# Performance work log

Hardware: AMD Instinct MI355X
Metric: run time of the kernel (lower is better)

The kernel has to match this reference:

```python
import jax, jax.numpy as jnp
import numpy as np

N_HEAD = 8
HEAD_DIM = 128
WINDOW = 512
ROPE_BASE = 10000.0


def _rope_tables(T, dtype):
    # inv_freq: [head_dim/2]
    inv_freq = 1.0 / (ROPE_BASE ** (jnp.arange(0, HEAD_DIM, 2, dtype=jnp.float32) / HEAD_DIM))
    t = jnp.arange(T, dtype=jnp.float32)
    freqs = jnp.einsum('i,j->ij', t, inv_freq)          # [T, head_dim/2]
    emb = jnp.concatenate([freqs, freqs], axis=-1)       # [T, head_dim]
    return jnp.cos(emb).astype(dtype), jnp.sin(emb).astype(dtype)


def _rotate_half(x):
    d = x.shape[-1] // 2
    return jnp.concatenate([-x[..., d:], x[..., :d]], axis=-1)


def setup_inputs() -> dict:
    key = jax.random.key(0)
    k1, k2, k3 = jax.random.split(key, 3)
    B, T, C = 2, 4096, 1024
    x = jax.random.normal(k1, (B, T, C), dtype=jnp.float32)
    w_qkv = jax.random.normal(k2, (3 * C, C), dtype=jnp.float32) * (1.0 / np.sqrt(C))
    w_o = jax.random.normal(k3, (C, C), dtype=jnp.float32) * (1.0 / np.sqrt(C))
    return {"x": x, "w_qkv": w_qkv, "w_o": w_o}


def reference(x, w_qkv, w_o):
    B, T, C = x.shape
    scale = 1.0 / np.sqrt(HEAD_DIM)
    qkv = x @ w_qkv.T                                     # [B,T,3C]
    q, k, v = jnp.split(qkv, 3, axis=-1)
    # [B, H, T, D]
    q = q.reshape(B, T, N_HEAD, HEAD_DIM).transpose(0, 2, 1, 3)
    k = k.reshape(B, T, N_HEAD, HEAD_DIM).transpose(0, 2, 1, 3)
    v = v.reshape(B, T, N_HEAD, HEAD_DIM).transpose(0, 2, 1, 3)
    cos, sin = _rope_tables(T, x.dtype)                   # [T, D]
    cos = cos[None, None]
    sin = sin[None, None]
    q = q * cos + _rotate_half(q) * sin
    k = k * cos + _rotate_half(k) * sin
    attn = jnp.einsum('bhqd,bhkd->bhqk', q, k) * scale    # [B,H,T,T]
    i = jnp.arange(T)[:, None]
    j = jnp.arange(T)[None, :]
    # causal (j<=i) AND sliding window triu(diag=-W) (j >= i - W)
    keep = (j <= i) & (j >= i - WINDOW)
    neg = jnp.finfo(attn.dtype).min
    attn = jnp.where(keep[None, None], attn, neg)
    attn = jax.nn.softmax(attn, axis=-1)
    out = jnp.einsum('bhqk,bhkd->bhqd', attn, v)          # [B,H,T,D]
    out = out.transpose(0, 2, 1, 3).reshape(B, T, C)
    return out @ w_o.T
```

## Files before the change

kernel.cpp:

```cpp
#include <hip/hip_runtime.h>
#include <hip/hip_bf16.h>

typedef unsigned short us;
typedef __attribute__((ext_vector_type(8))) __bf16 bf16x8;
typedef __attribute__((ext_vector_type(4))) float f32x4;

#define MFMA16(a, b, c) __builtin_amdgcn_mfma_f32_16x16x32_bf16(a, b, c, 0, 0, 0)

static __device__ __forceinline__ us f2bf(float f) {
  __hip_bfloat16 h = __float2bfloat16(f);
  return __builtin_bit_cast(us, h);
}

static __device__ __forceinline__ void gll16(const us* g, us* l) {
  __builtin_amdgcn_global_load_lds((const __attribute__((address_space(1))) void*)g,
                                   (__attribute__((address_space(3))) void*)l,
                                   16, 0, 0);
}

__global__ void cast_kernel(const float* __restrict__ in, us* __restrict__ out, int n4) {
  int i = blockIdx.x * blockDim.x + threadIdx.x;
  if (i >= n4) return;
  float4 v = ((const float4*)in)[i];
  ushort4 o;
  o.x = f2bf(v.x); o.y = f2bf(v.y); o.z = f2bf(v.z); o.w = f2bf(v.w);
  ((ushort4*)out)[i] = o;
}

__global__ void rope_table_kernel(float* __restrict__ ct, float* __restrict__ st) {
  int t = blockIdx.x, d = threadIdx.x;
  float ang = (float)t * exp2f((float)d * -0.20762050593046014f);
  float s, c;
  sincosf(ang, &s, &c);
  ct[t * 64 + d] = c;
  st[t * 64 + d] = s;
}

__global__ __launch_bounds__(256, 2)
void qkv_rope_kernel(const us* __restrict__ A, const us* __restrict__ B,
                     const float* __restrict__ ctab, const float* __restrict__ stab,
                     us* __restrict__ qb, us* __restrict__ kb, us* __restrict__ vtb) {
  __shared__ __align__(16) char smem_raw[128 * 132 * 4];
  us* sA = (us*)smem_raw;
  us* sB = sA + 128 * 64;
  float* sC = (float*)smem_raw;

  const int tid = threadIdx.x;
  const int lane = tid & 63;
  const int wave = tid >> 6;
  const int l15 = lane & 15;
  const int lq = lane >> 4;
  const int m0 = blockIdx.x * 128;
  const int n0 = blockIdx.y * 128;
  const int wm = (wave & 1) * 64;
  const int wn = (wave >> 1) * 64;

  f32x4 acc[4][4] = {};

  for (int k0 = 0; k0 < 1024; k0 += 64) {
    for (int i = 0; i < 4; ++i) {
      int c = wave * 4 + i;
      int P = c * 64 + lane;
      int row = P >> 3;
      int cb = (P & 7) ^ (row & 7);
      gll16(A + (size_t)(m0 + row) * 1024 + k0 + cb * 8, sA + c * 512);
      gll16(B + (size_t)(n0 + row) * 1024 + k0 + cb * 8, sB + c * 512);
    }
    __syncthreads();
#pragma unroll
    for (int kk = 0; kk < 64; kk += 32) {
      const int cbr = (kk + lq * 8) >> 3;
      bf16x8 av[4], bv[4];
#pragma unroll
      for (int mt = 0; mt < 4; ++mt) {
        int m = wm + mt * 16 + l15;
        av[mt] = *(const bf16x8*)(sA + (m * 8 + (cbr ^ (m & 7))) * 8);
      }
#pragma unroll
      for (int nt = 0; nt < 4; ++nt) {
        int n = wn + nt * 16 + l15;
        bv[nt] = *(const bf16x8*)(sB + (n * 8 + (cbr ^ (n & 7))) * 8);
      }
#pragma unroll
      for (int mt = 0; mt < 4; ++mt)
#pragma unroll
        for (int nt = 0; nt < 4; ++nt)
          acc[mt][nt] = MFMA16(av[mt], bv[nt], acc[mt][nt]);
    }
    __syncthreads();
  }

#pragma unroll
  for (int mt = 0; mt < 4; ++mt)
#pragma unroll
    for (int nt = 0; nt < 4; ++nt)
#pragma unroll
      for (int r = 0; r < 4; ++r) {
        int row = wm + mt * 16 + lq * 4 + r;
        int col = wn + nt * 16 + l15;
        sC[row * 132 + col] = acc[mt][nt][r];
      }
  __syncthreads();

  const int b = m0 >> 12;
  const int t0 = m0 & 4095;
  const int which = blockIdx.y >> 3;
  const int h = blockIdx.y & 7;

  if (which < 2) {
    us* outp = (which == 0) ? qb : kb;
    for (int r = 0; r < 8; ++r) {
      int tl = (tid >> 4) + r * 16;
      int d0 = (tid & 15) * 8;
      int tg = t0 + tl;
      int dm = d0 & 63;
      float cs[8], sn[8];
      *(float4*)(cs)     = *(const float4*)(ctab + tg * 64 + dm);
      *(float4*)(cs + 4) = *(const float4*)(ctab + tg * 64 + dm + 4);
      *(float4*)(sn)     = *(const float4*)(stab + tg * 64 + dm);
      *(float4*)(sn + 4) = *(const float4*)(stab + tg * 64 + dm + 4);
      union { us u[8]; uint4 v; } tmp;
#pragma unroll
      for (int j = 0; j < 8; ++j) {
        int d = d0 + j;
        float xv = sC[tl * 132 + d];
        float xp = sC[tl * 132 + (d ^ 64)];
        float rot = (d < 64) ? -xp : xp;
        tmp.u[j] = f2bf(xv * cs[j] + rot * sn[j]);
      }
      *(uint4*)(outp + ((size_t)((b * 8 + h) * 4096 + tg)) * 128 + d0) = tmp.v;
    }
  } else {
    for (int r = 0; r < 8; ++r) {
      int d = (tid >> 4) + r * 16;
      int tl0 = (tid & 15) * 8;
      union { us u[8]; uint4 v; } tmp;
#pragma unroll
      for (int j = 0; j < 8; ++j)
        tmp.u[j] = f2bf(sC[(tl0 + j) * 132 + d]);
      *(uint4*)(vtb + ((size_t)((b * 8 + h) * 128 + d)) * 4096 + t0 + tl0) = tmp.v;
    }
  }
}

template <int MASK>
__device__ __forceinline__ void softmax_step(f32x4 (&s)[8], f32x4 (&o)[8],
                                             float (&m_st)[4], float (&l_st)[4],
                                             us* __restrict__ sP,
                                             int t0, int tj0, int wm16, int lq, int l15) {
  const float C2 = 0.08838834764831845f * 1.4426950408889634f;
#pragma unroll
  for (int r = 0; r < 4; ++r) {
    const int rowl = wm16 + lq * 4 + r;
    const int ig = t0 + rowl;
    float mx = -3.0e38f;
#pragma unroll
    for (int nt = 0; nt < 8; ++nt) {
      float v = s[nt][r];
      if (MASK == 1) { int jg = tj0 + nt * 16 + l15; v = (jg + 512 >= ig) ? v : -3.0e38f; }
      if (MASK == 2) { int jg = tj0 + nt * 16 + l15; v = (jg <= ig) ? v : -3.0e38f; }
      s[nt][r] = v;
      mx = fmaxf(mx, v);
    }
#pragma unroll
    for (int off = 1; off < 16; off <<= 1) mx = fmaxf(mx, __shfl_xor(mx, off, 64));
    const float mold = m_st[r];
    const float mnew = fmaxf(mold, mx);
    const float alpha = exp2f((mold - mnew) * C2);
    float rs = 0.0f;
#pragma unroll
    for (int nt = 0; nt < 8; ++nt) {
      float p = exp2f((s[nt][r] - mnew) * C2);
      sP[rowl * 136 + nt * 16 + l15] = f2bf(p);
      rs += p;
    }
#pragma unroll
    for (int off = 1; off < 16; off <<= 1) rs += __shfl_xor(rs, off, 64);
    m_st[r] = mnew;
    l_st[r] = l_st[r] * alpha + rs;
#pragma unroll
    for (int dt = 0; dt < 8; ++dt) o[dt][r] *= alpha;
  }
}

__global__ __launch_bounds__(256, 2)
void flash_kernel(const us* __restrict__ qg, const us* __restrict__ kg,
                  const us* __restrict__ vg, us* __restrict__ ao) {
  __shared__ us sKP[128 * 128];
  __shared__ us sV[128 * 128];

  const int tid = threadIdx.x;
  const int lane = tid & 63;
  const int wave = tid >> 6;
  const int l15 = lane & 15;
  const int lq = lane >> 4;
  const int qx = blockIdx.x;
  const int h = blockIdx.y;
  const int b = blockIdx.z;
  const int t0 = qx * 64;
  const size_t bh = (size_t)(b * 8 + h);
  const int wm16 = wave * 16;

  bf16x8 qf[4];
#pragma unroll
  for (int ks = 0; ks < 4; ++ks)
    qf[ks] = *(const bf16x8*)(qg + (bh * 4096 + t0 + wm16 + l15) * 128 + ks * 32 + lq * 8);

  float m_st[4], l_st[4];
  f32x4 o[8] = {};
#pragma unroll
  for (int r = 0; r < 4; ++r) { m_st[r] = -3.0e38f; l_st[r] = 0.0f; }

  const int lo = t0 - 512;
  const int jtmin = (lo <= 0) ? 0 : (lo >> 7);
  const int jtmax = (t0 + 63) >> 7;
  const bool wmask = (t0 >= 512);

  for (int jt = jtmin; jt <= jtmax; ++jt) {
    const int tj0 = jt * 128;
    for (int i = 0; i < 8; ++i) {
      int c = wave * 8 + i;
      int P = c * 64 + lane;
      int row = P >> 4;
      int cb = (P & 15) ^ (row & 15);
      gll16(kg + (bh * 4096 + tj0 + row) * 128 + cb * 8, sKP + c * 512);
      gll16(vg + (bh * 128 + row) * 4096 + tj0 + cb * 8, sV + c * 512);
    }
    __syncthreads();

    f32x4 s[8] = {};
#pragma unroll
    for (int ks = 0; ks < 4; ++ks) {
      const int cbr = ks * 4 + lq;
#pragma unroll
      for (int nt = 0; nt < 8; ++nt) {
        int n = nt * 16 + l15;
        bf16x8 bk = *(const bf16x8*)(sKP + (n * 16 + (cbr ^ (n & 15))) * 8);
        s[nt] = MFMA16(qf[ks], bk, s[nt]);
      }
    }
    __syncthreads();

    if (jt == jtmax)               softmax_step<2>(s, o, m_st, l_st, sKP, t0, tj0, wm16, lq, l15);
    else if (wmask && jt == jtmin) softmax_step<1>(s, o, m_st, l_st, sKP, t0, tj0, wm16, lq, l15);
    else                           softmax_step<0>(s, o, m_st, l_st, sKP, t0, tj0, wm16, lq, l15);

#pragma unroll
    for (int ks = 0; ks < 4; ++ks) {
      const int ko = ks * 32 + lq * 8;
      const int cbr = ko >> 3;
      bf16x8 ap = *(const bf16x8*)(sKP + (wm16 + l15) * 136 + ko);
#pragma unroll
      for (int dt = 0; dt < 8; ++dt) {
        int dd = dt * 16 + l15;
        bf16x8 bv = *(const bf16x8*)(sV + (dd * 16 + (cbr ^ (dd & 15))) * 8);
        o[dt] = MFMA16(ap, bv, o[dt]);
      }
    }
    __syncthreads();
  }

#pragma unroll
  for (int r = 0; r < 4; ++r) {
    const float inv = 1.0f / l_st[r];
    const int rowl = wm16 + lq * 4 + r;
    const size_t base = ((size_t)b * 4096 + t0 + rowl) * 1024 + h * 128;
#pragma unroll
    for (int dt = 0; dt < 8; ++dt)
      ao[base + dt * 16 + l15] = f2bf(o[dt][r] * inv);
  }
}

__global__ __launch_bounds__(256, 2)
void out_proj_kernel(const us* __restrict__ A, const us* __restrict__ B, float* __restrict__ C) {
  __shared__ us sA[128 * 64];
  __shared__ us sB[128 * 64];
  const int tid = threadIdx.x;
  const int lane = tid & 63;
  const int wave = tid >> 6;
  const int l15 = lane & 15;
  const int lq = lane >> 4;
  const int m0 = blockIdx.x * 128;
  const int n0 = blockIdx.y * 128;
  const int wm = (wave & 1) * 64;
  const int wn = (wave >> 1) * 64;
  f32x4 acc[4][4] = {};
  for (int k0 = 0; k0 < 1024; k0 += 64) {
    for (int i = 0; i < 4; ++i) {
      int c = wave * 4 + i;
      int P = c * 64 + lane;
      int row = P >> 3;
      int cb = (P & 7) ^ (row & 7);
      gll16(A + (size_t)(m0 + row) * 1024 + k0 + cb * 8, sA + c * 512);
      gll16(B + (size_t)(n0 + row) * 1024 + k0 + cb * 8, sB + c * 512);
    }
    __syncthreads();
#pragma unroll
    for (int kk = 0; kk < 64; kk += 32) {
      const int cbr = (kk + lq * 8) >> 3;
      bf16x8 av[4], bv[4];
#pragma unroll
      for (int mt = 0; mt < 4; ++mt) {
        int m = wm + mt * 16 + l15;
        av[mt] = *(const bf16x8*)(sA + (m * 8 + (cbr ^ (m & 7))) * 8);
      }
#pragma unroll
      for (int nt = 0; nt < 4; ++nt) {
        int n = wn + nt * 16 + l15;
        bv[nt] = *(const bf16x8*)(sB + (n * 8 + (cbr ^ (n & 7))) * 8);
      }
#pragma unroll
      for (int mt = 0; mt < 4; ++mt)
#pragma unroll
        for (int nt = 0; nt < 4; ++nt)
          acc[mt][nt] = MFMA16(av[mt], bv[nt], acc[mt][nt]);
    }
    __syncthreads();
  }
#pragma unroll
  for (int mt = 0; mt < 4; ++mt)
#pragma unroll
    for (int nt = 0; nt < 4; ++nt)
#pragma unroll
      for (int r = 0; r < 4; ++r)
        C[(size_t)(m0 + wm + mt * 16 + lq * 4 + r) * 1024 + (n0 + wn + nt * 16 + l15)] =
            acc[mt][nt][r];
}

extern "C" void kernel_launch(void* const* d_in, const int* in_sizes, int n_in,
                              void* d_out, int out_size, void* d_ws, size_t ws_size,
                              hipStream_t stream) {
  const float* x     = (const float*)d_in[0];
  const float* w_qkv = (const float*)d_in[1];
  const float* w_o   = (const float*)d_in[2];
  float* out = (float*)d_out;

  us* xb  = (us*)d_ws;
  us* wqb = xb  + (size_t)8192 * 1024;
  us* wob = wqb + (size_t)3072 * 1024;
  us* qb  = wob + (size_t)1024 * 1024;
  us* kb  = qb  + (size_t)2 * 8 * 4096 * 128;
  us* vtb = kb  + (size_t)2 * 8 * 4096 * 128;
  us* aob = vtb + (size_t)2 * 8 * 4096 * 128;
  float* ctab = (float*)(aob + (size_t)8192 * 1024);
  float* stab = ctab + (size_t)4096 * 64;

  rope_table_kernel<<<4096, 64, 0, stream>>>(ctab, stab);
  cast_kernel<<<8192, 256, 0, stream>>>(x, xb, 8192 * 1024 / 4);
  cast_kernel<<<3072, 256, 0, stream>>>(w_qkv, wqb, 3072 * 1024 / 4);
  cast_kernel<<<1024, 256, 0, stream>>>(w_o, wob, 1024 * 1024 / 4);
  qkv_rope_kernel<<<dim3(64, 24), 256, 0, stream>>>(xb, wqb, ctab, stab, qb, kb, vtb);
  flash_kernel<<<dim3(64, 8, 2), 256, 0, stream>>>(qb, kb, vtb, aob);
  out_proj_kernel<<<dim3(64, 8), 256, 0, stream>>>(aob, wob, out);
}
```

Baseline: 248.1 us.

## Apply RoPE from registers in QKV epilogue and shrink flash KV tile to 64

In the QKV GEMM epilogue the column mapping per wave is remapped so each lane holds both rotate-half partners (d and d^64) in registers. RoPE is then applied straight from the accumulators, which drops the LDS round trip and barrier for Q and K; V still goes through LDS with a padded 129 stride for the transpose. The flash kernel cuts the KV tile from 128 to 64 keys, halving shared memory, and raises launch bounds to 4 blocks per CU so occupancy is higher and fewer fully masked keys are processed near the causal and window edges. In exchange there are twice as many loop iterations and barriers, and the Q/K epilogue stores become narrow scalar bf16 writes instead of 16-byte vector writes.

```diff
diff --git a/kernel.cpp b/kernel.cpp
--- a/kernel.cpp
+++ b/kernel.cpp
@@ -53,7 +53,7 @@
   const int m0 = blockIdx.x * 128;
   const int n0 = blockIdx.y * 128;
   const int wm = (wave & 1) * 64;
-  const int wn = (wave >> 1) * 64;
+  const int wn2 = (wave >> 1) * 32;
 
   f32x4 acc[4][4] = {};
 
@@ -78,7 +78,7 @@
       }
 #pragma unroll
       for (int nt = 0; nt < 4; ++nt) {
-        int n = wn + nt * 16 + l15;
+        int n = wn2 + (nt & 1) * 16 + (nt >> 1) * 64 + l15;
         bv[nt] = *(const bf16x8*)(sB + (n * 8 + (cbr ^ (n & 7))) * 8);
       }
 #pragma unroll
@@ -89,18 +89,6 @@
     }
     __syncthreads();
   }
-
-#pragma unroll
-  for (int mt = 0; mt < 4; ++mt)
-#pragma unroll
-    for (int nt = 0; nt < 4; ++nt)
-#pragma unroll
-      for (int r = 0; r < 4; ++r) {
-        int row = wm + mt * 16 + lq * 4 + r;
-        int col = wn + nt * 16 + l15;
-        sC[row * 132 + col] = acc[mt][nt][r];
-      }
-  __syncthreads();
 
   const int b = m0 >> 12;
   const int t0 = m0 & 4095;
@@ -109,42 +97,51 @@
 
   if (which < 2) {
     us* outp = (which == 0) ? qb : kb;
-    for (int r = 0; r < 8; ++r) {
-      int tl = (tid >> 4) + r * 16;
-      int d0 = (tid & 15) * 8;
-      int tg = t0 + tl;
-      int dm = d0 & 63;
-      float cs[8], sn[8];
-      *(float4*)(cs)     = *(const float4*)(ctab + tg * 64 + dm);
-      *(float4*)(cs + 4) = *(const float4*)(ctab + tg * 64 + dm + 4);
-      *(float4*)(sn)     = *(const float4*)(stab + tg * 64 + dm);
-      *(float4*)(sn + 4) = *(const float4*)(stab + tg * 64 + dm + 4);
-      union { us u[8]; uint4 v; } tmp;
-#pragma unroll
-      for (int j = 0; j < 8; ++j) {
-        int d = d0 + j;
-        float xv = sC[tl * 132 + d];
-        float xp = sC[tl * 132 + (d ^ 64)];
-        float rot = (d < 64) ? -xp : xp;
-        tmp.u[j] = f2bf(xv * cs[j] + rot * sn[j]);
-      }
-      *(uint4*)(outp + ((size_t)((b * 8 + h) * 4096 + tg)) * 128 + d0) = tmp.v;
-    }
+    const size_t obase = ((size_t)(b * 8 + h)) * 4096 * 128;
+#pragma unroll
+    for (int mt = 0; mt < 4; ++mt)
+#pragma unroll
+      for (int r = 0; r < 4; ++r) {
+        const int row = wm + mt * 16 + lq * 4 + r;
+        const int tg = t0 + row;
+        const float* cp = ctab + tg * 64 + wn2 + l15;
+        const float* sp = stab + tg * 64 + wn2 + l15;
+        const float c0 = cp[0], c1 = cp[16], s0 = sp[0], s1 = sp[16];
+        us* orow = outp + obase + (size_t)tg * 128 + wn2 + l15;
+#pragma unroll
+        for (int nt = 0; nt < 4; ++nt) {
+          float x = acc[mt][nt][r];
+          float xp = acc[mt][nt ^ 2][r];
+          float rot = (nt < 2) ? -xp : xp;
+          float y = x * ((nt & 1) ? c1 : c0) + rot * ((nt & 1) ? s1 : s0);
+          orow[(nt & 1) * 16 + (nt >> 1) * 64] = f2bf(y);
+        }
+      }
   } else {
+#pragma unroll
+    for (int mt = 0; mt < 4; ++mt)
+#pragma unroll
+      for (int nt = 0; nt < 4; ++nt) {
+        const int col = wn2 + (nt & 1) * 16 + (nt >> 1) * 64 + l15;
+#pragma unroll
+        for (int r = 0; r < 4; ++r)
+          sC[(wm + mt * 16 + lq * 4 + r) * 129 + col] = acc[mt][nt][r];
+      }
+    __syncthreads();
     for (int r = 0; r < 8; ++r) {
       int d = (tid >> 4) + r * 16;
       int tl0 = (tid & 15) * 8;
       union { us u[8]; uint4 v; } tmp;
 #pragma unroll
       for (int j = 0; j < 8; ++j)
-        tmp.u[j] = f2bf(sC[(tl0 + j) * 132 + d]);
+        tmp.u[j] = f2bf(sC[(tl0 + j) * 129 + d]);
       *(uint4*)(vtb + ((size_t)((b * 8 + h) * 128 + d)) * 4096 + t0 + tl0) = tmp.v;
     }
   }
 }
 
 template <int MASK>
-__device__ __forceinline__ void softmax_step(f32x4 (&s)[8], f32x4 (&o)[8],
+__device__ __forceinline__ void softmax_step(f32x4 (&s)[4], f32x4 (&o)[8],
                                              float (&m_st)[4], float (&l_st)[4],
                                              us* __restrict__ sP,
                                              int t0, int tj0, int wm16, int lq, int l15) {
@@ -155,7 +152,7 @@
     const int ig = t0 + rowl;
     float mx = -3.0e38f;
 #pragma unroll
-    for (int nt = 0; nt < 8; ++nt) {
+    for (int nt = 0; nt < 4; ++nt) {
       float v = s[nt][r];
       if (MASK == 1) { int jg = tj0 + nt * 16 + l15; v = (jg + 512 >= ig) ? v : -3.0e38f; }
       if (MASK == 2) { int jg = tj0 + nt * 16 + l15; v = (jg <= ig) ? v : -3.0e38f; }
@@ -169,9 +166,9 @@
     const float alpha = exp2f((mold - mnew) * C2);
     float rs = 0.0f;
 #pragma unroll
-    for (int nt = 0; nt < 8; ++nt) {
+    for (int nt = 0; nt < 4; ++nt) {
       float p = exp2f((s[nt][r] - mnew) * C2);
-      sP[rowl * 136 + nt * 16 + l15] = f2bf(p);
+      sP[rowl * 72 + nt * 16 + l15] = f2bf(p);
       rs += p;
     }
 #pragma unroll
@@ -183,11 +180,11 @@
   }
 }
 
-__global__ __launch_bounds__(256, 2)
+__global__ __launch_bounds__(256, 4)
 void flash_kernel(const us* __restrict__ qg, const us* __restrict__ kg,
                   const us* __restrict__ vg, us* __restrict__ ao) {
-  __shared__ us sKP[128 * 128];
-  __shared__ us sV[128 * 128];
+  __shared__ us sKP[64 * 128];
+  __shared__ us sV[128 * 64];
 
   const int tid = threadIdx.x;
   const int lane = tid & 63;
@@ -212,28 +209,30 @@
   for (int r = 0; r < 4; ++r) { m_st[r] = -3.0e38f; l_st[r] = 0.0f; }
 
   const int lo = t0 - 512;
-  const int jtmin = (lo <= 0) ? 0 : (lo >> 7);
-  const int jtmax = (t0 + 63) >> 7;
+  const int jtmin = (lo <= 0) ? 0 : (lo >> 6);
+  const int jtmax = t0 >> 6;
   const bool wmask = (t0 >= 512);
 
   for (int jt = jtmin; jt <= jtmax; ++jt) {
-    const int tj0 = jt * 128;
-    for (int i = 0; i < 8; ++i) {
-      int c = wave * 8 + i;
+    const int tj0 = jt * 64;
+    for (int i = 0; i < 4; ++i) {
+      int c = wave * 4 + i;
       int P = c * 64 + lane;
-      int row = P >> 4;
-      int cb = (P & 15) ^ (row & 15);
-      gll16(kg + (bh * 4096 + tj0 + row) * 128 + cb * 8, sKP + c * 512);
-      gll16(vg + (bh * 128 + row) * 4096 + tj0 + cb * 8, sV + c * 512);
-    }
-    __syncthreads();
-
-    f32x4 s[8] = {};
+      int rowK = P >> 4;
+      int cbK = (P & 15) ^ (rowK & 15);
+      gll16(kg + (bh * 4096 + tj0 + rowK) * 128 + cbK * 8, sKP + c * 512);
+      int rowV = P >> 3;
+      int cbV = (P & 7) ^ (rowV & 7);
+      gll16(vg + (bh * 128 + rowV) * 4096 + tj0 + cbV * 8, sV + c * 512);
+    }
+    __syncthreads();
+
+    f32x4 s[4] = {};
 #pragma unroll
     for (int ks = 0; ks < 4; ++ks) {
       const int cbr = ks * 4 + lq;
 #pragma unroll
-      for (int nt = 0; nt < 8; ++nt) {
+      for (int nt = 0; nt < 4; ++nt) {
         int n = nt * 16 + l15;
         bf16x8 bk = *(const bf16x8*)(sKP + (n * 16 + (cbr ^ (n & 15))) * 8);
         s[nt] = MFMA16(qf[ks], bk, s[nt]);
@@ -246,14 +245,14 @@
     else                           softmax_step<0>(s, o, m_st, l_st, sKP, t0, tj0, wm16, lq, l15);
 
 #pragma unroll
-    for (int ks = 0; ks < 4; ++ks) {
+    for (int ks = 0; ks < 2; ++ks) {
       const int ko = ks * 32 + lq * 8;
-      const int cbr = ko >> 3;
-      bf16x8 ap = *(const bf16x8*)(sKP + (wm16 + l15) * 136 + ko);
+      const int slot = ks * 4 + lq;
+      bf16x8 ap = *(const bf16x8*)(sKP + (wm16 + l15) * 72 + ko);
 #pragma unroll
       for (int dt = 0; dt < 8; ++dt) {
         int dd = dt * 16 + l15;
-        bf16x8 bv = *(const bf16x8*)(sV + (dd * 16 + (cbr ^ (dd & 15))) * 8);
+        bf16x8 bv = *(const bf16x8*)(sV + (dd * 8 + (slot ^ (dd & 7))) * 8);
         o[dt] = MFMA16(ap, bv, o[dt]);
       }
     }
```

New measurement: 309.4 us. 1.25x slower.
